# Kernel tuning notes

Measured on AMD Instinct MI355X. Metric: run time of the kernel, lower is better.

The kernel has to match this reference:

```python
import jax, jax.numpy as jnp
import numpy as np

NEG_SLOPE = 0.01  # F.leaky_relu default
N_NODES = 50000
N_EDGES = 800000
DIMS = [1, 64, 128, 64, 1]


def _lrelu(x):
    return jnp.where(x >= 0, x, NEG_SLOPE * x)


def _gconv(x, src, dst, W, b, n):
    # DGL GraphConv, norm='none': sum-aggregate src features into dst, then linear.
    # (DGL multiplies first when in_feats > out_feats; identical math since sum is linear.)
    if x.shape[1] > W.shape[1]:
        x = x @ W
        return jax.ops.segment_sum(x[src], dst, num_segments=n) + b
    agg = jax.ops.segment_sum(x[src], dst, num_segments=n)  # [n, d_in]
    return agg @ W + b


def setup_inputs() -> dict:
    key = jax.random.key(0)
    ks = jax.random.split(key, 16)
    inp = {
        "in_feat": jax.random.normal(ks[0], (N_NODES, 1), jnp.float32),
        "src": jax.random.randint(ks[1], (N_EDGES,), 0, N_NODES),
        "dst": jax.random.randint(ks[2], (N_EDGES,), 0, N_NODES),
    }
    for i in range(4):
        fi, fo = DIMS[i], DIMS[i + 1]
        scale = (2.0 / (fi + fo)) ** 0.5  # xavier-style
        inp[f"W{i}"] = jax.random.normal(ks[3 + 2 * i], (fi, fo), jnp.float32) * scale
        inp[f"b{i}"] = jax.random.normal(ks[4 + 2 * i], (fo,), jnp.float32) * 0.01
    return inp


def reference(in_feat, src, dst, W0, b0, W1, b1, W2, b2, W3, b3):
    n = in_feat.shape[0]
    h = _lrelu(_gconv(in_feat, src, dst, W0, b0, n))
    h = _lrelu(_gconv(h, src, dst, W1, b1, n))
    h = _lrelu(_gconv(h, src, dst, W2, b2, n))
    h = _lrelu(_gconv(h, src, dst, W3, b3, n))
    return h[1]  # node index 1, shape (1,)
```

## Files before the change

kernel.cpp:

```cpp
#include <hip/hip_runtime.h>

#define N_NODES 50000
#define N_EDGES 800000
#define NE4 (N_EDGES / 4)
#define NMASKW 1568
#define MAXN1 192
#define S2MAX 1024
#define DMAX  4096
#define E1MAX 1024
#define BK    96
#define SB   ((NE4 + 255) / 256)
#define FGRID 256
#define SUBN 8
#define SUBW 64

#define AS(p, v) __hip_atomic_store((p), (v), __ATOMIC_RELAXED, __HIP_MEMORY_SCOPE_AGENT)

__device__ __forceinline__ float lrelu(float v) { return v >= 0.f ? v : 0.01f * v; }
__device__ __forceinline__ bool mtest(const unsigned int* m, int i) {
    return (m[i >> 5] >> (i & 31)) & 1u;
}

__global__ __launch_bounds__(256) void scan1_k(const int4* __restrict__ dst4,
                                               const int* __restrict__ src,
                                               unsigned int* __restrict__ f1m,
                                               int* __restrict__ e1src, int* __restrict__ cntE1,
                                               int* __restrict__ pos1, int* __restrict__ cnt1) {
    int t = blockIdx.x * 256 + threadIdx.x;
    if (t >= NE4) return;
    int4 d4 = dst4[t];
#define E1(dd, off) \
    if (dd == 1) { \
        int ss = src[t * 4 + off]; \
        int q = atomicAdd(cntE1, 1); \
        if (q < E1MAX) AS(&e1src[q], ss); \
        unsigned int bit = 1u << (ss & 31); \
        unsigned int old = atomicOr(&f1m[ss >> 5], bit); \
        if (!(old & bit)) { int q1 = atomicAdd(cnt1, 1); AS(&pos1[ss], q1); } }
    E1(d4.x, 0) E1(d4.y, 1) E1(d4.z, 2) E1(d4.w, 3)
#undef E1
}

__global__ __launch_bounds__(256) void scan2_k(const int4* __restrict__ dst4,
                                               const int* __restrict__ src,
                                               const unsigned int* __restrict__ f1m,
                                               unsigned int* __restrict__ f2m,
                                               const int* __restrict__ pos1,
                                               int* __restrict__ pos2, int* __restrict__ cnt2,
                                               int2* __restrict__ eD, int* __restrict__ cntD) {
    __shared__ unsigned int msk[NMASKW];
    for (int k = threadIdx.x; k < NMASKW; k += 256) msk[k] = f1m[k];
    __syncthreads();
    int t = blockIdx.x * 256 + threadIdx.x;
    if (t >= NE4) return;
    int4 d4 = dst4[t];
#define E2(dd, off) \
    if (mtest(msk, dd)) { \
        int ss = src[t * 4 + off]; \
        unsigned int bit = 1u << (ss & 31); \
        unsigned int old = atomicOr(&f2m[ss >> 5], bit); \
        if (!(old & bit)) { int q2 = atomicAdd(cnt2, 1); if (q2 < S2MAX) AS(&pos2[ss], q2); } \
        int q = atomicAdd(cntD, 1); \
        if (q < DMAX) { \
            unsigned long long ev = (unsigned long long)(unsigned int)ss | \
                ((unsigned long long)(unsigned int)pos1[dd] << 32); \
            AS((unsigned long long*)&eD[q], ev); } }
    E2(d4.x, 0) E2(d4.y, 1) E2(d4.z, 2) E2(d4.w, 3)
#undef E2
}

__global__ __launch_bounds__(256) void scan3_k(const int4* __restrict__ dst4,
                                               const int* __restrict__ src,
                                               const unsigned int* __restrict__ f2m,
                                               unsigned int* __restrict__ f3m,
                                               const int* __restrict__ pos2,
                                               float* __restrict__ agg0,
                                               int* __restrict__ bucket,
                                               int* __restrict__ slotCnt) {
    __shared__ unsigned int msk[NMASKW];
    for (int k = threadIdx.x; k < NMASKW; k += 256) msk[k] = f2m[k];
    __syncthreads();
    int t = blockIdx.x * 256 + threadIdx.x;
    if (t >= NE4) return;
    int4 d4 = dst4[t];
#define E3(dd, off) \
    if (mtest(msk, dd)) { \
        int ss = src[t * 4 + off]; \
        unsigned int bit = 1u << (ss & 31); \
        unsigned int old = atomicOr(&f3m[ss >> 5], bit); \
        if (!(old & bit)) AS(&agg0[ss], 0.f); \
        int sl = pos2[dd]; \
        if ((unsigned)sl < S2MAX) { \
            int bi = atomicAdd(&slotCnt[sl], 1); \
            if (bi < BK) AS(&bucket[sl * BK + bi], ss); } }
    E3(d4.x, 0) E3(d4.y, 1) E3(d4.z, 2) E3(d4.w, 3)
#undef E3
}

__global__ __launch_bounds__(256) void scan4_k(const int4* __restrict__ dst4,
                                               const int4* __restrict__ src4,
                                               const float* __restrict__ x,
                                               const unsigned int* __restrict__ f3m,
                                               float* __restrict__ agg0,
                                               const int2* __restrict__ eD,
                                               const int* __restrict__ cntD,
                                               const int* __restrict__ pos2,
                                               int2* __restrict__ eDr) {
    __shared__ unsigned int msk[NMASKW];
    int g = blockIdx.x * 256 + threadIdx.x;
    {
        int cD = *cntD; if (cD > DMAX) cD = DMAX;
        if (g < cD) {
            int2 e = eD[g];
            int sl = pos2[e.x];
            unsigned long long ev =
                (unsigned long long)(unsigned int)((unsigned)sl < S2MAX ? sl : -1) |
                ((unsigned long long)(unsigned int)e.y << 32);
            AS((unsigned long long*)&eDr[g], ev);
        }
    }
    for (int k = threadIdx.x; k < NMASKW; k += 256) msk[k] = f3m[k];
    __syncthreads();
    int t = g;
    if (t >= NE4) return;
    int4 d4 = dst4[t];
    bool m0 = mtest(msk, d4.x), m1 = mtest(msk, d4.y);
    bool m2 = mtest(msk, d4.z), m3 = mtest(msk, d4.w);
    if (m0 | m1 | m2 | m3) {
        int4 s4 = src4[t];
        if (m0) atomicAdd(&agg0[d4.x], x[s4.x]);
        if (m1) atomicAdd(&agg0[d4.y], x[s4.y]);
        if (m2) atomicAdd(&agg0[d4.z], x[s4.z]);
        if (m3) atomicAdd(&agg0[d4.w], x[s4.w]);
    }
}

struct P7 {
    const int* bucket; const int* slotCnt; const float* agg0;
    const float* W0; const float* b0; const float* W1; const float* b1;
    const float* W2; const float* b2; const float* W3; const float* b3;
    const int* cnt2; const int* pos1;
    const int2* eDr; const int* cntD; const int* e1src; const int* cntE1;
    const int* cnt1; float* gacc; int* sub; int* top; float* out;
};

__global__ __launch_bounds__(256) void fused7_k(P7 p) {
    __shared__ float xv[128];
    __shared__ float part[256];
    __shared__ float rowA[64];
    __shared__ float rowH[128];
    __shared__ float rowT[64];
    __shared__ float t3s[MAXN1];
    __shared__ int lflag;
    const int tid = threadIdx.x;
    const int g = tid >> 6, j = tid & 63;
    int c2 = *p.cnt2; if (c2 > S2MAX) c2 = S2MAX;
    int cD = *p.cntD; if (cD > DMAX) cD = DMAX;
    const float w0 = p.W0[j], bb0 = p.b0[j];

    for (int b = blockIdx.x; b < c2; b += FGRID) {
        int cnt = p.slotCnt[b]; if (cnt > BK) cnt = BK;
        if (tid < cnt) xv[tid] = p.agg0[p.bucket[b * BK + tid]];
        __syncthreads();
        float racc = 0.f;
        for (int m = g; m < cnt; m += 4) racc += lrelu(xv[m] * w0 + bb0);
        part[tid] = racc;
        __syncthreads();
        if (tid < 64)
            rowA[tid] = part[tid] + part[64 + tid] + part[128 + tid] + part[192 + tid];
        __syncthreads();
        if (tid < 128) {
            float h = p.b1[tid];
#pragma unroll
            for (int k = 0; k < 64; ++k) h += rowA[k] * p.W1[k * 128 + tid];
            rowH[tid] = lrelu(h);
        }
        __syncthreads();
        if (tid < 64) {
            float a2 = 0.f;
#pragma unroll
            for (int k = 0; k < 128; ++k) a2 += rowH[k] * p.W2[k * 64 + tid];
            rowT[tid] = a2;
        }
        __syncthreads();
        for (int base = 0; base < cD; base += 256) {
            int i = base + tid;
            int2 e = make_int2(-1, -1);
            if (i < cD) e = p.eDr[i];
            bool m = (e.x == b);
            unsigned long long bal = __ballot(m);
            while (bal) {
                int bit = __builtin_ctzll(bal); bal &= bal - 1;
                int sl1 = __shfl(e.y, bit, 64);
                if ((unsigned)sl1 < MAXN1)
                    atomicAdd(&p.gacc[sl1 * 64 + j], rowT[j]);
            }
        }
        __syncthreads();
    }

    __syncthreads();
    if (tid == 0) {
        lflag = 0;
        int s = blockIdx.x & (SUBN - 1);
        int old = __hip_atomic_fetch_add(&p.sub[s * SUBW], 1,
                                         __ATOMIC_RELAXED, __HIP_MEMORY_SCOPE_AGENT);
        if (old == (FGRID / SUBN) - 1) {
            int o2 = __hip_atomic_fetch_add(p.top, 1,
                                            __ATOMIC_RELAXED, __HIP_MEMORY_SCOPE_AGENT);
            lflag = (o2 == SUBN - 1);
        }
    }
    __syncthreads();
    if (!lflag) return;

    {
        int c1 = *p.cnt1;  if (c1 > MAXN1) c1 = MAXN1;
        int cE = *p.cntE1; if (cE > E1MAX) cE = E1MAX;
        int widx = tid >> 6;
        for (int slot = widx; slot < c1; slot += 4) {
            float v = lrelu(p.gacc[slot * 64 + j] + p.b2[j]) * p.W3[j];
            for (int off = 32; off > 0; off >>= 1) v += __shfl_down(v, off, 64);
            if (j == 0) t3s[slot] = v;
        }
        __syncthreads();
        if (tid < 64) {
            float ssum = 0.f;
            for (int k = tid; k < cE; k += 64) ssum += t3s[p.pos1[p.e1src[k]]];
            for (int off = 32; off > 0; off >>= 1) ssum += __shfl_down(ssum, off, 64);
            if (tid == 0) p.out[0] = lrelu(ssum + p.b3[0]);
        }
    }
}

extern "C" void kernel_launch(void* const* d_in, const int* in_sizes, int n_in,
                              void* d_out, int out_size, void* d_ws, size_t ws_size,
                              hipStream_t stream) {
    const float* x   = (const float*)d_in[0];
    const int*   src = (const int*)d_in[1];
    const int*   dst = (const int*)d_in[2];
    const float* W0 = (const float*)d_in[3];  const float* b0 = (const float*)d_in[4];
    const float* W1 = (const float*)d_in[5];  const float* b1 = (const float*)d_in[6];
    const float* W2 = (const float*)d_in[7];  const float* b2 = (const float*)d_in[8];
    const float* W3 = (const float*)d_in[9];  const float* b3 = (const float*)d_in[10];
    float* out = (float*)d_out;
    const int4* dst4 = (const int4*)dst;
    const int4* src4 = (const int4*)src;

    char* base = (char*)d_ws;
    size_t off = 0;
    auto take = [&](size_t bytes) { char* q = base + off; off += (bytes + 255) & ~(size_t)255; return q; };
    unsigned int* f1m = (unsigned int*)take(NMASKW * 4);
    unsigned int* f2m = (unsigned int*)take(NMASKW * 4);
    unsigned int* f3m = (unsigned int*)take(NMASKW * 4);
    int* cntE1 = (int*)take(4);
    int* cntD  = (int*)take(4);
    int* cnt1  = (int*)take(4);
    int* cnt2  = (int*)take(4);
    int* slotCnt = (int*)take((size_t)S2MAX * 4);
    int* sub   = (int*)take((size_t)SUBN * SUBW * 4);
    int* top   = (int*)take(4);
    float* gacc = (float*)take((size_t)MAXN1 * 64 * 4);
    size_t zero_bytes = off;
    float* agg0   = (float*)take((size_t)N_NODES * 4);
    int*   e1src  = (int*)take((size_t)E1MAX * 4);
    int2*  eD     = (int2*)take((size_t)DMAX * 8);
    int2*  eDr    = (int2*)take((size_t)DMAX * 8);
    int*   bucket = (int*)take((size_t)S2MAX * BK * 4);
    int*   pos1   = (int*)take((size_t)N_NODES * 4);
    int*   pos2   = (int*)take((size_t)N_NODES * 4);

    hipMemsetAsync(base, 0, zero_bytes, stream);

    scan1_k<<<SB, 256, 0, stream>>>(dst4, src, f1m, e1src, cntE1, pos1, cnt1);
    scan2_k<<<SB, 256, 0, stream>>>(dst4, src, f1m, f2m, pos1, pos2, cnt2, eD, cntD);
    scan3_k<<<SB, 256, 0, stream>>>(dst4, src, f2m, f3m, pos2, agg0, bucket, slotCnt);
    scan4_k<<<SB, 256, 0, stream>>>(dst4, src4, x, f3m, agg0, eD, cntD, pos2, eDr);

    P7 hp;
    hp.bucket = bucket; hp.slotCnt = slotCnt; hp.agg0 = agg0;
    hp.W0 = W0; hp.b0 = b0; hp.W1 = W1; hp.b1 = b1;
    hp.W2 = W2; hp.b2 = b2; hp.W3 = W3; hp.b3 = b3;
    hp.cnt2 = cnt2; hp.pos1 = pos1;
    hp.eDr = eDr; hp.cntD = cntD; hp.e1src = e1src; hp.cntE1 = cntE1;
    hp.cnt1 = cnt1; hp.gacc = gacc; hp.sub = sub; hp.top = top; hp.out = out;
    fused7_k<<<FGRID, 256, 0, stream>>>(hp);
}
```

Measured before the change: 128.8 us.

## Drop memset and scan4 launch; fuse layer-0 gather into final kernel with grid barrier

```diff
diff --git a/kernel.cpp b/kernel.cpp
--- a/kernel.cpp
+++ b/kernel.cpp
@@ -4,17 +4,18 @@
 #define N_EDGES 800000
 #define NE4 (N_EDGES / 4)
 #define NMASKW 1568
-#define MAXN1 192
+#define C1MAX 64
+#define CAP   16
 #define S2MAX 1024
 #define DMAX  4096
-#define E1MAX 1024
 #define BK    96
-#define SB   ((NE4 + 255) / 256)
+#define SB1   ((NE4 + 255) / 256)
 #define FGRID 256
-#define SUBN 8
-#define SUBW 64
-
-#define AS(p, v) __hip_atomic_store((p), (v), __ATOMIC_RELAXED, __HIP_MEMORY_SCOPE_AGENT)
+#define SUBW  64
+
+#define AS(p, v)  __hip_atomic_store((p), (v), __ATOMIC_RELAXED, __HIP_MEMORY_SCOPE_AGENT)
+#define ALD(p)    __hip_atomic_load((p), __ATOMIC_RELAXED, __HIP_MEMORY_SCOPE_AGENT)
+#define AADD(p,v) __hip_atomic_fetch_add((p), (v), __ATOMIC_RELAXED, __HIP_MEMORY_SCOPE_AGENT)
 
 __device__ __forceinline__ float lrelu(float v) { return v >= 0.f ? v : 0.01f * v; }
 __device__ __forceinline__ bool mtest(const unsigned int* m, int i) {
@@ -23,50 +24,82 @@
 
 __global__ __launch_bounds__(256) void scan1_k(const int4* __restrict__ dst4,
                                                const int* __restrict__ src,
-                                               unsigned int* __restrict__ f1m,
-                                               int* __restrict__ e1src, int* __restrict__ cntE1,
-                                               int* __restrict__ pos1, int* __restrict__ cnt1) {
-    int t = blockIdx.x * 256 + threadIdx.x;
-    if (t >= NE4) return;
-    int4 d4 = dst4[t];
-#define E1(dd, off) \
-    if (dd == 1) { \
-        int ss = src[t * 4 + off]; \
-        int q = atomicAdd(cntE1, 1); \
-        if (q < E1MAX) AS(&e1src[q], ss); \
-        unsigned int bit = 1u << (ss & 31); \
-        unsigned int old = atomicOr(&f1m[ss >> 5], bit); \
-        if (!(old & bit)) { int q1 = atomicAdd(cnt1, 1); AS(&pos1[ss], q1); } }
-    E1(d4.x, 0) E1(d4.y, 1) E1(d4.z, 2) E1(d4.w, 3)
-#undef E1
+                                               int* __restrict__ e1cnt, int* __restrict__ e1val,
+                                               unsigned int* __restrict__ zbase, int zwords) {
+    __shared__ int lcnt;
+    __shared__ int lval[CAP];
+    const int tid = threadIdx.x;
+    const int t = blockIdx.x * 256 + tid;
+    if (tid == 0) lcnt = 0;
+    __syncthreads();
+    if (t < zwords) zbase[t] = 0u;
+    if (t < NE4) {
+        int4 d4 = dst4[t];
+        int dv[4] = { d4.x, d4.y, d4.z, d4.w };
+#pragma unroll
+        for (int k = 0; k < 4; ++k) {
+            if (dv[k] == 1) {
+                int q = atomicAdd(&lcnt, 1);
+                if (q < CAP) lval[q] = src[t * 4 + k];
+            }
+        }
+    }
+    __syncthreads();
+    int c = lcnt < CAP ? lcnt : CAP;
+    if (tid == 0) e1cnt[blockIdx.x] = c;
+    if (tid < c) e1val[blockIdx.x * CAP + tid] = lval[tid];
 }
 
 __global__ __launch_bounds__(256) void scan2_k(const int4* __restrict__ dst4,
                                                const int* __restrict__ src,
-                                               const unsigned int* __restrict__ f1m,
+                                               const int* __restrict__ e1cnt,
+                                               const int* __restrict__ e1val,
                                                unsigned int* __restrict__ f2m,
-                                               const int* __restrict__ pos1,
                                                int* __restrict__ pos2, int* __restrict__ cnt2,
                                                int2* __restrict__ eD, int* __restrict__ cntD) {
     __shared__ unsigned int msk[NMASKW];
-    for (int k = threadIdx.x; k < NMASKW; k += 256) msk[k] = f1m[k];
-    __syncthreads();
-    int t = blockIdx.x * 256 + threadIdx.x;
+    __shared__ int candN[C1MAX];
+    __shared__ int candC;
+    const int tid = threadIdx.x;
+    for (int k = tid; k < NMASKW; k += 256) msk[k] = 0u;
+    if (tid == 0) candC = 0;
+    __syncthreads();
+    for (int b = tid; b < SB1; b += 256) {
+        int c = e1cnt[b]; if (c > CAP) c = CAP;
+        for (int i = 0; i < c; ++i) {
+            int n = e1val[b * CAP + i];
+            unsigned int bit = 1u << (n & 31);
+            unsigned int old = atomicOr(&msk[n >> 5], bit);
+            if (!(old & bit)) { int q = atomicAdd(&candC, 1); if (q < C1MAX) candN[q] = n; }
+        }
+    }
+    __syncthreads();
+    int c1 = candC; if (c1 > C1MAX) c1 = C1MAX;
+    int t = blockIdx.x * 256 + tid;
     if (t >= NE4) return;
     int4 d4 = dst4[t];
-#define E2(dd, off) \
-    if (mtest(msk, dd)) { \
-        int ss = src[t * 4 + off]; \
-        unsigned int bit = 1u << (ss & 31); \
-        unsigned int old = atomicOr(&f2m[ss >> 5], bit); \
-        if (!(old & bit)) { int q2 = atomicAdd(cnt2, 1); if (q2 < S2MAX) AS(&pos2[ss], q2); } \
-        int q = atomicAdd(cntD, 1); \
-        if (q < DMAX) { \
-            unsigned long long ev = (unsigned long long)(unsigned int)ss | \
-                ((unsigned long long)(unsigned int)pos1[dd] << 32); \
-            AS((unsigned long long*)&eD[q], ev); } }
-    E2(d4.x, 0) E2(d4.y, 1) E2(d4.z, 2) E2(d4.w, 3)
-#undef E2
+    int dv[4] = { d4.x, d4.y, d4.z, d4.w };
+#pragma unroll
+    for (int k = 0; k < 4; ++k) {
+        int dd = dv[k];
+        if (mtest(msk, dd)) {
+            int ss = src[t * 4 + k];
+            unsigned int bit = 1u << (ss & 31);
+            unsigned int old = atomicOr(&f2m[ss >> 5], bit);
+            if (!(old & bit)) {
+                int q2 = atomicAdd(cnt2, 1);
+                if (q2 < S2MAX) AS(&pos2[ss], q2);
+            }
+            int r = 0;
+            for (int u = 0; u < c1; ++u) r += (candN[u] < dd);
+            int q = atomicAdd(cntD, 1);
+            if (q < DMAX) {
+                unsigned long long ev = (unsigned long long)(unsigned int)ss |
+                                        ((unsigned long long)(unsigned int)r << 32);
+                AS((unsigned long long*)&eD[q], ev);
+            }
+        }
+    }
 }
 
 __global__ __launch_bounds__(256) void scan3_k(const int4* __restrict__ dst4,
@@ -78,86 +111,93 @@
                                                int* __restrict__ bucket,
                                                int* __restrict__ slotCnt) {
     __shared__ unsigned int msk[NMASKW];
-    for (int k = threadIdx.x; k < NMASKW; k += 256) msk[k] = f2m[k];
-    __syncthreads();
-    int t = blockIdx.x * 256 + threadIdx.x;
+    const int tid = threadIdx.x;
+    for (int k = tid; k < NMASKW; k += 256) msk[k] = f2m[k];
+    __syncthreads();
+    int t = blockIdx.x * 256 + tid;
     if (t >= NE4) return;
     int4 d4 = dst4[t];
-#define E3(dd, off) \
-    if (mtest(msk, dd)) { \
-        int ss = src[t * 4 + off]; \
-        unsigned int bit = 1u << (ss & 31); \
-        unsigned int old = atomicOr(&f3m[ss >> 5], bit); \
-        if (!(old & bit)) AS(&agg0[ss], 0.f); \
-        int sl = pos2[dd]; \
-        if ((unsigned)sl < S2MAX) { \
-            int bi = atomicAdd(&slotCnt[sl], 1); \
-            if (bi < BK) AS(&bucket[sl * BK + bi], ss); } }
-    E3(d4.x, 0) E3(d4.y, 1) E3(d4.z, 2) E3(d4.w, 3)
-#undef E3
-}
-
-__global__ __launch_bounds__(256) void scan4_k(const int4* __restrict__ dst4,
-                                               const int4* __restrict__ src4,
-                                               const float* __restrict__ x,
-                                               const unsigned int* __restrict__ f3m,
-                                               float* __restrict__ agg0,
-                                               const int2* __restrict__ eD,
-                                               const int* __restrict__ cntD,
-                                               const int* __restrict__ pos2,
-                                               int2* __restrict__ eDr) {
-    __shared__ unsigned int msk[NMASKW];
-    int g = blockIdx.x * 256 + threadIdx.x;
-    {
-        int cD = *cntD; if (cD > DMAX) cD = DMAX;
-        if (g < cD) {
-            int2 e = eD[g];
-            int sl = pos2[e.x];
-            unsigned long long ev =
-                (unsigned long long)(unsigned int)((unsigned)sl < S2MAX ? sl : -1) |
-                ((unsigned long long)(unsigned int)e.y << 32);
-            AS((unsigned long long*)&eDr[g], ev);
-        }
-    }
-    for (int k = threadIdx.x; k < NMASKW; k += 256) msk[k] = f3m[k];
-    __syncthreads();
-    int t = g;
-    if (t >= NE4) return;
-    int4 d4 = dst4[t];
-    bool m0 = mtest(msk, d4.x), m1 = mtest(msk, d4.y);
-    bool m2 = mtest(msk, d4.z), m3 = mtest(msk, d4.w);
-    if (m0 | m1 | m2 | m3) {
-        int4 s4 = src4[t];
-        if (m0) atomicAdd(&agg0[d4.x], x[s4.x]);
-        if (m1) atomicAdd(&agg0[d4.y], x[s4.y]);
-        if (m2) atomicAdd(&agg0[d4.z], x[s4.z]);
-        if (m3) atomicAdd(&agg0[d4.w], x[s4.w]);
-    }
-}
-
-struct P7 {
-    const int* bucket; const int* slotCnt; const float* agg0;
+    int dv[4] = { d4.x, d4.y, d4.z, d4.w };
+#pragma unroll
+    for (int k = 0; k < 4; ++k) {
+        int dd = dv[k];
+        if (mtest(msk, dd)) {
+            int ss = src[t * 4 + k];
+            unsigned int bit = 1u << (ss & 31);
+            unsigned int old = atomicOr(&f3m[ss >> 5], bit);
+            if (!(old & bit)) AS(&agg0[ss], 0.f);
+            int sl = pos2[dd];
+            if ((unsigned)sl < S2MAX) {
+                int bi = atomicAdd(&slotCnt[sl], 1);
+                if (bi < BK) AS(&bucket[sl * BK + bi], ss);
+            }
+        }
+    }
+}
+
+struct P8 {
+    const int4* dst4; const int4* src4; const float* x;
+    const unsigned int* f3m; float* agg0;
+    const int2* eD; const int* cntD; const int* pos2; int2* eDr;
+    const int* bucket; const int* slotCnt; const int* cnt2;
+    const int* e1cnt; const int* e1val;
     const float* W0; const float* b0; const float* W1; const float* b1;
     const float* W2; const float* b2; const float* W3; const float* b3;
-    const int* cnt2; const int* pos1;
-    const int2* eDr; const int* cntD; const int* e1src; const int* cntE1;
-    const int* cnt1; float* gacc; int* sub; int* top; float* out;
+    float* gacc; int* sub; int* top; int* rel; int* subB; int* topB; float* out;
 };
 
-__global__ __launch_bounds__(256) void fused7_k(P7 p) {
+__global__ __launch_bounds__(256) void fused8_k(P8 p) {
+    __shared__ unsigned int msk[NMASKW];
     __shared__ float xv[128];
     __shared__ float part[256];
     __shared__ float rowA[64];
     __shared__ float rowH[128];
     __shared__ float rowT[64];
-    __shared__ float t3s[MAXN1];
+    __shared__ float t3s[C1MAX];
+    __shared__ int candN[C1MAX];
+    __shared__ int candC;
     __shared__ int lflag;
     const int tid = threadIdx.x;
+    const int gid = blockIdx.x * 256 + tid;
     const int g = tid >> 6, j = tid & 63;
+
+    int cD = *p.cntD; if (cD > DMAX) cD = DMAX;
+    if (gid < cD) {
+        int2 e = p.eD[gid];
+        int sl = p.pos2[e.x];
+        unsigned long long ev =
+            (unsigned long long)(unsigned int)((unsigned)sl < S2MAX ? sl : -1) |
+            ((unsigned long long)(unsigned int)e.y << 32);
+        AS((unsigned long long*)&p.eDr[gid], ev);
+    }
+    for (int k = tid; k < NMASKW; k += 256) msk[k] = p.f3m[k];
+    __syncthreads();
+    for (int t = gid; t < NE4; t += FGRID * 256) {
+        int4 d4 = p.dst4[t];
+        bool m0 = mtest(msk, d4.x), m1 = mtest(msk, d4.y);
+        bool m2 = mtest(msk, d4.z), m3 = mtest(msk, d4.w);
+        if (m0 | m1 | m2 | m3) {
+            int4 s4 = p.src4[t];
+            if (m0) atomicAdd(&p.agg0[d4.x], p.x[s4.x]);
+            if (m1) atomicAdd(&p.agg0[d4.y], p.x[s4.y]);
+            if (m2) atomicAdd(&p.agg0[d4.z], p.x[s4.z]);
+            if (m3) atomicAdd(&p.agg0[d4.w], p.x[s4.w]);
+        }
+    }
+    __syncthreads();
+    if (tid == 0) {
+        int s = blockIdx.x & 7;
+        int old = AADD(&p.sub[s * SUBW], 1);
+        if (old == (FGRID / 8) - 1) {
+            int o2 = AADD(p.top, 1);
+            if (o2 == 7) AS(p.rel, 1);
+        }
+        while (ALD(p.rel) == 0) __builtin_amdgcn_s_sleep(8);
+    }
+    __syncthreads();
+
     int c2 = *p.cnt2; if (c2 > S2MAX) c2 = S2MAX;
-    int cD = *p.cntD; if (cD > DMAX) cD = DMAX;
     const float w0 = p.W0[j], bb0 = p.b0[j];
-
     for (int b = blockIdx.x; b < c2; b += FGRID) {
         int cnt = p.slotCnt[b]; if (cnt > BK) cnt = BK;
         if (tid < cnt) xv[tid] = p.agg0[p.bucket[b * BK + tid]];
@@ -192,7 +232,7 @@
             while (bal) {
                 int bit = __builtin_ctzll(bal); bal &= bal - 1;
                 int sl1 = __shfl(e.y, bit, 64);
-                if ((unsigned)sl1 < MAXN1)
+                if ((unsigned)sl1 < C1MAX)
                     atomicAdd(&p.gacc[sl1 * 64 + j], rowT[j]);
             }
         }
@@ -202,35 +242,57 @@
     __syncthreads();
     if (tid == 0) {
         lflag = 0;
-        int s = blockIdx.x & (SUBN - 1);
-        int old = __hip_atomic_fetch_add(&p.sub[s * SUBW], 1,
-                                         __ATOMIC_RELAXED, __HIP_MEMORY_SCOPE_AGENT);
-        if (old == (FGRID / SUBN) - 1) {
-            int o2 = __hip_atomic_fetch_add(p.top, 1,
-                                            __ATOMIC_RELAXED, __HIP_MEMORY_SCOPE_AGENT);
-            lflag = (o2 == SUBN - 1);
+        int s = blockIdx.x & 7;
+        int old = AADD(&p.subB[s * SUBW], 1);
+        if (old == (FGRID / 8) - 1) {
+            int o2 = AADD(p.topB, 1);
+            lflag = (o2 == 7);
         }
     }
     __syncthreads();
     if (!lflag) return;
 
-    {
-        int c1 = *p.cnt1;  if (c1 > MAXN1) c1 = MAXN1;
-        int cE = *p.cntE1; if (cE > E1MAX) cE = E1MAX;
-        int widx = tid >> 6;
-        for (int slot = widx; slot < c1; slot += 4) {
-            float v = lrelu(p.gacc[slot * 64 + j] + p.b2[j]) * p.W3[j];
-            for (int off = 32; off > 0; off >>= 1) v += __shfl_down(v, off, 64);
-            if (j == 0) t3s[slot] = v;
-        }
-        __syncthreads();
-        if (tid < 64) {
-            float ssum = 0.f;
-            for (int k = tid; k < cE; k += 64) ssum += t3s[p.pos1[p.e1src[k]]];
-            for (int off = 32; off > 0; off >>= 1) ssum += __shfl_down(ssum, off, 64);
-            if (tid == 0) p.out[0] = lrelu(ssum + p.b3[0]);
-        }
-    }
+    for (int k = tid; k < NMASKW; k += 256) msk[k] = 0u;
+    if (tid == 0) candC = 0;
+    __syncthreads();
+    for (int b = tid; b < SB1; b += 256) {
+        int c = p.e1cnt[b]; if (c > CAP) c = CAP;
+        for (int i = 0; i < c; ++i) {
+            int n = p.e1val[b * CAP + i];
+            unsigned int bit = 1u << (n & 31);
+            unsigned int old = atomicOr(&msk[n >> 5], bit);
+            if (!(old & bit)) { int q = atomicAdd(&candC, 1); if (q < C1MAX) candN[q] = n; }
+        }
+    }
+    __syncthreads();
+    int c1 = candC; if (c1 > C1MAX) c1 = C1MAX;
+    int widx = tid >> 6;
+    for (int q = widx; q < c1; q += 4) {
+        int n = candN[q];
+        int r = 0;
+        for (int u = 0; u < c1; ++u) r += (candN[u] < n);
+        float v = lrelu(p.gacc[r * 64 + j] + p.b2[j]) * p.W3[j];
+        for (int off = 32; off > 0; off >>= 1) v += __shfl_down(v, off, 64);
+        if (j == 0) t3s[r] = v;
+    }
+    __syncthreads();
+    float ssum = 0.f;
+    for (int b = tid; b < SB1; b += 256) {
+        int c = p.e1cnt[b]; if (c > CAP) c = CAP;
+        for (int i = 0; i < c; ++i) {
+            int n = p.e1val[b * CAP + i];
+            int r = 0;
+            for (int u = 0; u < c1; ++u) r += (candN[u] < n);
+            ssum += t3s[r];
+        }
+    }
+    part[tid] = ssum;
+    __syncthreads();
+    for (int off = 128; off > 0; off >>= 1) {
+        if (tid < off) part[tid] += part[tid + off];
+        __syncthreads();
+    }
+    if (tid == 0) p.out[0] = lrelu(part[0] + p.b3[0]);
 }
 
 extern "C" void kernel_launch(void* const* d_in, const int* in_sizes, int n_in,
@@ -250,39 +312,39 @@
     char* base = (char*)d_ws;
     size_t off = 0;
     auto take = [&](size_t bytes) { char* q = base + off; off += (bytes + 255) & ~(size_t)255; return q; };
-    unsigned int* f1m = (unsigned int*)take(NMASKW * 4);
     unsigned int* f2m = (unsigned int*)take(NMASKW * 4);
     unsigned int* f3m = (unsigned int*)take(NMASKW * 4);
-    int* cntE1 = (int*)take(4);
+    int* cnt2  = (int*)take(4);
     int* cntD  = (int*)take(4);
-    int* cnt1  = (int*)take(4);
-    int* cnt2  = (int*)take(4);
+    int* top   = (int*)take(4);
+    int* rel   = (int*)take(4);
+    int* topB  = (int*)take(4);
+    int* sub   = (int*)take((size_t)8 * SUBW * 4);
+    int* subB  = (int*)take((size_t)8 * SUBW * 4);
     int* slotCnt = (int*)take((size_t)S2MAX * 4);
-    int* sub   = (int*)take((size_t)SUBN * SUBW * 4);
-    int* top   = (int*)take(4);
-    float* gacc = (float*)take((size_t)MAXN1 * 64 * 4);
-    size_t zero_bytes = off;
+    float* gacc  = (float*)take((size_t)C1MAX * 64 * 4);
+    int zwords = (int)(off / 4);
     float* agg0   = (float*)take((size_t)N_NODES * 4);
-    int*   e1src  = (int*)take((size_t)E1MAX * 4);
+    int*   e1cnt  = (int*)take((size_t)SB1 * 4);
+    int*   e1val  = (int*)take((size_t)SB1 * CAP * 4);
     int2*  eD     = (int2*)take((size_t)DMAX * 8);
     int2*  eDr    = (int2*)take((size_t)DMAX * 8);
     int*   bucket = (int*)take((size_t)S2MAX * BK * 4);
-    int*   pos1   = (int*)take((size_t)N_NODES * 4);
     int*   pos2   = (int*)take((size_t)N_NODES * 4);
 
-    hipMemsetAsync(base, 0, zero_bytes, stream);
-
-    scan1_k<<<SB, 256, 0, stream>>>(dst4, src, f1m, e1src, cntE1, pos1, cnt1);
-    scan2_k<<<SB, 256, 0, stream>>>(dst4, src, f1m, f2m, pos1, pos2, cnt2, eD, cntD);
-    scan3_k<<<SB, 256, 0, stream>>>(dst4, src, f2m, f3m, pos2, agg0, bucket, slotCnt);
-    scan4_k<<<SB, 256, 0, stream>>>(dst4, src4, x, f3m, agg0, eD, cntD, pos2, eDr);
-
-    P7 hp;
-    hp.bucket = bucket; hp.slotCnt = slotCnt; hp.agg0 = agg0;
+    scan1_k<<<SB1, 256, 0, stream>>>(dst4, src, e1cnt, e1val, (unsigned int*)base, zwords);
+    scan2_k<<<SB1, 256, 0, stream>>>(dst4, src, e1cnt, e1val, f2m, pos2, cnt2, eD, cntD);
+    scan3_k<<<SB1, 256, 0, stream>>>(dst4, src, f2m, f3m, pos2, agg0, bucket, slotCnt);
+
+    P8 hp;
+    hp.dst4 = dst4; hp.src4 = src4; hp.x = x;
+    hp.f3m = f3m; hp.agg0 = agg0;
+    hp.eD = eD; hp.cntD = cntD; hp.pos2 = pos2; hp.eDr = eDr;
+    hp.bucket = bucket; hp.slotCnt = slotCnt; hp.cnt2 = cnt2;
+    hp.e1cnt = e1cnt; hp.e1val = e1val;
     hp.W0 = W0; hp.b0 = b0; hp.W1 = W1; hp.b1 = b1;
     hp.W2 = W2; hp.b2 = b2; hp.W3 = W3; hp.b3 = b3;
-    hp.cnt2 = cnt2; hp.pos1 = pos1;
-    hp.eDr = eDr; hp.cntD = cntD; hp.e1src = e1src; hp.cntE1 = cntE1;
-    hp.cnt1 = cnt1; hp.gacc = gacc; hp.sub = sub; hp.top = top; hp.out = out;
-    fused7_k<<<FGRID, 256, 0, stream>>>(hp);
-}
+    hp.gacc = gacc; hp.sub = sub; hp.top = top; hp.rel = rel;
+    hp.subB = subB; hp.topB = topB; hp.out = out;
+    fused8_k<<<FGRID, 256, 0, stream>>>(hp);
+}
```

After: 139.4 us. 1.08x slower.
